# Kernel optimization log

Measured on AMD Instinct MI355X. Metric: run time of the kernel, lower is better.

Reference implementation:

```python
import jax, jax.numpy as jnp
import numpy as np

N = 50000
E = 1600000
IN_CH = 34
HID = 64
OUT = 64
NEG_SLOPE = 0.2


def _gat_layer(x, src, dst, W, a_src, a_dst, bias, heads, out_ch, concat):
    n = x.shape[0]
    xw = (x @ W).reshape(n, heads, out_ch)                      # [N,H,C]
    al_src = jnp.sum(xw * a_src[None], axis=-1)                  # [N,H]
    al_dst = jnp.sum(xw * a_dst[None], axis=-1)                  # [N,H]
    e = jax.nn.leaky_relu(al_src[src] + al_dst[dst], NEG_SLOPE)  # [E,H]
    # segment softmax over incoming edges of each dst node (self-loops ensure non-empty)
    m = jax.ops.segment_max(e, dst, num_segments=n)              # [N,H]
    ex = jnp.exp(e - m[dst])
    denom = jax.ops.segment_sum(ex, dst, num_segments=n)         # [N,H]
    alpha = ex / denom[dst]                                      # [E,H]
    msg = xw[src] * alpha[:, :, None]                            # [E,H,C]
    out = jax.ops.segment_sum(msg, dst, num_segments=n)          # [N,H,C]
    if concat:
        out = out.reshape(n, heads * out_ch)
    else:
        out = out.mean(axis=1)
    return out + bias


def setup_inputs() -> dict:
    key = jax.random.key(0)
    ks = jax.random.split(key, 12)
    x = jax.random.normal(ks[0], (N, IN_CH), dtype=jnp.float32)
    edge_index = jax.random.randint(ks[1], (2, E), 0, N, dtype=jnp.int64)
    # layer 1: heads=2, concat -> 128
    W1 = jax.random.normal(ks[2], (IN_CH, 2 * HID), dtype=jnp.float32) * 0.1
    a_src1 = jax.random.normal(ks[3], (2, HID), dtype=jnp.float32) * 0.1
    a_dst1 = jax.random.normal(ks[4], (2, HID), dtype=jnp.float32) * 0.1
    b1 = jnp.zeros((2 * HID,), dtype=jnp.float32)
    # layer 2: heads=1, mean
    W2 = jax.random.normal(ks[5], (2 * HID, OUT), dtype=jnp.float32) * 0.1
    a_src2 = jax.random.normal(ks[6], (1, OUT), dtype=jnp.float32) * 0.1
    a_dst2 = jax.random.normal(ks[7], (1, OUT), dtype=jnp.float32) * 0.1
    b2 = jnp.zeros((OUT,), dtype=jnp.float32)
    return {"x": x, "edge_index": edge_index, "W1": W1, "a_src1": a_src1,
            "a_dst1": a_dst1, "b1": b1, "W2": W2, "a_src2": a_src2,
            "a_dst2": a_dst2, "b2": b2}


def reference(x, edge_index, W1, a_src1, a_dst1, b1, W2, a_src2, a_dst2, b2):
    n = x.shape[0]
    loops = jnp.arange(n, dtype=edge_index.dtype)
    src = jnp.concatenate([edge_index[0], loops])  # PyG GATConv add_self_loops=True
    dst = jnp.concatenate([edge_index[1], loops])
    h = _gat_layer(x, src, dst, W1, a_src1, a_dst1, b1, heads=2, out_ch=HID, concat=True)
    h = jax.nn.relu(h)
    out = _gat_layer(h, src, dst, W2, a_src2, a_dst2, b2, heads=1, out_ch=OUT, concat=False)
    return out
```

## Files before the change

kernel.cpp:

```cpp
#include <hip/hip_runtime.h>
#include <math.h>

#define N_NODES 50000
#define E_EDGES 1600000
#define IN_CH   34
#define NEG     0.2f
#define NB      196
#define CAP     10000

typedef __attribute__((ext_vector_type(2))) float fv2;

static __device__ __forceinline__ unsigned short f2bf(float f) {
    unsigned int u = __float_as_uint(f);
    u += 0x7fffu + ((u >> 16) & 1u);
    return (unsigned short)(u >> 16);
}
static __device__ __forceinline__ float bflo(unsigned int u) {
    return __uint_as_float(u << 16);
}
static __device__ __forceinline__ float bfhi(unsigned int u) {
    return __uint_as_float(u & 0xffff0000u);
}
static __device__ __forceinline__ float lrelu_exp(float e) {
    return expf(e > 0.f ? e : NEG * e);
}

static __device__ __forceinline__ int scan256_excl(int v, int* wsum) {
    const int lane = threadIdx.x & 63, wv = threadIdx.x >> 6;
    int x = v;
    #pragma unroll
    for (int off = 1; off < 64; off <<= 1) {
        int y = __shfl_up(x, off);
        if (lane >= off) x += y;
    }
    if (lane == 63) wsum[wv] = x;
    __syncthreads();
    if (threadIdx.x < 4) {
        int s = wsum[threadIdx.x];
        #pragma unroll
        for (int off = 1; off < 4; off <<= 1) {
            int y = __shfl_up(s, off);
            if ((int)threadIdx.x >= off) s += y;
        }
        wsum[threadIdx.x] = s;
    }
    __syncthreads();
    const int woff = wv ? wsum[wv - 1] : 0;
    return woff + x - v;
}

__global__ __launch_bounds__(256) void k_bin(
    const int* __restrict__ srcA, const int* __restrict__ dstA,
    int* __restrict__ gcur, unsigned int* __restrict__ binned)
{
    __shared__ unsigned int raw[4096];
    __shared__ unsigned short rnk[4096];
    __shared__ int cnt[256], cur[256];
    const int tid = threadIdx.x;
    cnt[tid] = 0;
    __syncthreads();
    const int base = blockIdx.x * 4096;
    #pragma unroll
    for (int i = 0; i < 16; ++i) {
        const int e = base + i * 256 + tid;
        if (e < E_EDGES) {
            const int d = dstA[e], s = srcA[e];
            raw[i * 256 + tid] = ((unsigned int)d << 16) | (unsigned int)s;
            rnk[i * 256 + tid] = (unsigned short)atomicAdd(&cnt[d >> 8], 1);
        }
    }
    __syncthreads();
    const int v = cnt[tid];
    cur[tid] = (tid < NB && v > 0) ? (tid * CAP + atomicAdd(&gcur[tid], v)) : 0;
    __syncthreads();
    const int mE = min(4096, E_EDGES - base);
    for (int p = tid; p < mE; p += 256) {
        const unsigned int u = raw[p];
        binned[cur[u >> 24] + rnk[p]] = u;
    }
}

__global__ __launch_bounds__(256) void k_fine(
    const int* __restrict__ gcur, const unsigned int* __restrict__ binned,
    int2* __restrict__ rowspan, unsigned short* __restrict__ sorted_src)
{
    __shared__ unsigned int sbin[CAP];
    __shared__ unsigned short rnk[CAP];
    __shared__ int cnt[256], sbase[256];
    __shared__ int wsum[4];
    const int tid = threadIdx.x;
    const int b = blockIdx.x;
    const int bbase = b * CAP;
    const int cntb = gcur[b];
    cnt[tid] = 0;
    __syncthreads();
    for (int p = tid; p < cntb; p += 256) {
        const unsigned int u = binned[bbase + p];
        sbin[p] = u;
        rnk[p] = (unsigned short)atomicAdd(&cnt[(u >> 16) & 255], 1);
    }
    __syncthreads();
    const int v = cnt[tid];
    const int excl = scan256_excl(v, wsum);
    const int node = b * 256 + tid;
    if (node < N_NODES) rowspan[node] = make_int2(bbase + excl, bbase + excl + v);
    sbase[tid] = excl;
    __syncthreads();
    for (int p = tid; p < cntb; p += 256) {
        const unsigned int u = sbin[p];
        sorted_src[bbase + sbase[(u >> 16) & 255] + rnk[p]] =
            (unsigned short)(u & 0xffffu);
    }
}

__global__ __launch_bounds__(256) void k_node1(
    const float* __restrict__ x, const float* __restrict__ W1,
    const float* __restrict__ a_src, const float* __restrict__ a_dst,
    unsigned short* __restrict__ xw1b,
    float* __restrict__ al_s, float* __restrict__ al_d)
{
    __shared__ float sW[IN_CH * 132];
    __shared__ float sx[32 * 35];
    __shared__ float sas[128], sad[128];
    const int tid = threadIdx.x;
    for (int i = tid; i < IN_CH * 128; i += 256) {
        int k = i >> 7, c = i & 127;
        sW[k * 132 + c] = W1[i];
    }
    if (tid < 128) { sas[tid] = a_src[tid]; sad[tid] = a_dst[tid]; }
    const int n0 = blockIdx.x * 32;
    for (int i = tid; i < 32 * IN_CH; i += 256) {
        int n = i / IN_CH;
        sx[n * 35 + (i - n * IN_CH)] = (n0 + n < N_NODES) ? x[n0 * IN_CH + i] : 0.f;
    }
    __syncthreads();

    const int tc = tid & 31, tn = tid >> 5;
    float acc[4][4] = {{0.f}};
    for (int k = 0; k < IN_CH; ++k) {
        const float4 wv = *reinterpret_cast<const float4*>(&sW[k * 132 + 4 * tc]);
        #pragma unroll
        for (int j = 0; j < 4; ++j) {
            const float hj = sx[(4 * tn + j) * 35 + k];
            acc[j][0] += hj * wv.x; acc[j][1] += hj * wv.y;
            acc[j][2] += hj * wv.z; acc[j][3] += hj * wv.w;
        }
    }
    #pragma unroll
    for (int j = 0; j < 4; ++j) {
        const int node = n0 + 4 * tn + j;
        float ps = 0.f, pd = 0.f;
        #pragma unroll
        for (int c = 0; c < 4; ++c) {
            ps += acc[j][c] * sas[4 * tc + c];
            pd += acc[j][c] * sad[4 * tc + c];
        }
        #pragma unroll
        for (int off = 1; off < 16; off <<= 1) {
            ps += __shfl_xor(ps, off);
            pd += __shfl_xor(pd, off);
        }
        if (node < N_NODES) {
            if ((tc & 15) == 0) {
                int h = tc >> 4;
                al_s[node * 2 + h] = ps;
                al_d[node * 2 + h] = pd;
            }
            ushort4 u;
            u.x = f2bf(acc[j][0]); u.y = f2bf(acc[j][1]);
            u.z = f2bf(acc[j][2]); u.w = f2bf(acc[j][3]);
            *reinterpret_cast<ushort4*>(&xw1b[node * 128 + 4 * tc]) = u;
        }
    }
}

__global__ __launch_bounds__(256) void k_gather1(
    const int2* __restrict__ rowspan, const unsigned short* __restrict__ sorted_src,
    const unsigned int* __restrict__ xw1u,
    const float* __restrict__ al_s, const float* __restrict__ al_d,
    const float* __restrict__ b1, float* __restrict__ hbuf)
{
    __shared__ float4 AB[2][4][32];
    const int wave = threadIdx.x >> 6;
    const int lane = threadIdx.x & 63;
    const int node = blockIdx.x * 4 + wave;
    const int2 span = rowspan[node];
    const int head = lane >> 5;

    const float2 ald  = *reinterpret_cast<const float2*>(&al_d[node * 2]);
    const float2 als0 = *reinterpret_cast<const float2*>(&al_s[node * 2]);
    const float w0h0 = lrelu_exp(als0.x + ald.x);
    const float w0h1 = lrelu_exp(als0.y + ald.y);
    const float wself = head ? w0h1 : w0h0;

    const unsigned int su = xw1u[node * 64 + lane];
    fv2 accX = { wself * bflo(su), wself * bfhi(su) };
    fv2 accY = { 0.f, 0.f };
    float dv0 = 0.f, dv1 = 0.f;
    const float4* ABh = AB[head][wave];

    for (int base = span.x; base < span.y; base += 64) {
        const int rem = span.y - base;
        const int m = rem < 64 ? rem : 64;
        const int mp = (m + 1) & ~1;
        if (lane < m) {
            const int s = sorted_src[base + lane];
            const float2 als = *reinterpret_cast<const float2*>(&al_s[s * 2]);
            const float w0 = lrelu_exp(als.x + ald.x);
            const float w1 = lrelu_exp(als.y + ald.y);
            dv0 += w0; dv1 += w1;
            const float offf = __int_as_float(s << 6);
            ((float2*)&AB[0][wave][lane >> 1])[lane & 1] = make_float2(offf, w0);
            ((float2*)&AB[1][wave][lane >> 1])[lane & 1] = make_float2(offf, w1);
        } else if (lane < mp) {
            const float offf = __int_as_float(node << 6);
            ((float2*)&AB[0][wave][lane >> 1])[lane & 1] = make_float2(offf, 0.f);
            ((float2*)&AB[1][wave][lane >> 1])[lane & 1] = make_float2(offf, 0.f);
        }
        const int P = mp >> 1;
        int p = 0;
        for (; p + 8 <= P; p += 8) {
            float4 q[8];
            #pragma unroll
            for (int t = 0; t < 8; ++t) q[t] = ABh[p + t];
            unsigned int va[8], vb[8];
            #pragma unroll
            for (int t = 0; t < 8; ++t) {
                va[t] = xw1u[__float_as_int(q[t].x) + lane];
                vb[t] = xw1u[__float_as_int(q[t].z) + lane];
            }
            #pragma unroll
            for (int t = 0; t < 8; ++t) {
                fv2 f;
                f.x = bflo(va[t]); f.y = bfhi(va[t]); accX += f * q[t].y;
                f.x = bflo(vb[t]); f.y = bfhi(vb[t]); accY += f * q[t].w;
            }
        }
        for (; p < P; ++p) {
            const float4 q = ABh[p];
            const unsigned int a = xw1u[__float_as_int(q.x) + lane];
            const unsigned int b = xw1u[__float_as_int(q.z) + lane];
            fv2 f;
            f.x = bflo(a); f.y = bfhi(a); accX += f * q.y;
            f.x = bflo(b); f.y = bfhi(b); accY += f * q.w;
        }
    }
    accX += accY;
    #pragma unroll
    for (int off = 32; off; off >>= 1) {
        dv0 += __shfl_xor(dv0, off);
        dv1 += __shfl_xor(dv1, off);
    }
    const float den = head ? (dv1 + w0h1) : (dv0 + w0h0);
    const float2 bv = *reinterpret_cast<const float2*>(&b1[2 * lane]);
    float o0 = accX.x / den + bv.x;
    float o1 = accX.y / den + bv.y;
    o0 = o0 > 0.f ? o0 : 0.f;
    o1 = o1 > 0.f ? o1 : 0.f;
    *reinterpret_cast<float2*>(&hbuf[node * 128 + 2 * lane]) = make_float2(o0, o1);
}

__global__ __launch_bounds__(256) void k_node2(
    const float* __restrict__ hbuf, const float* __restrict__ W2,
    const float* __restrict__ a_src, const float* __restrict__ a_dst,
    unsigned short* __restrict__ xw2b, float* __restrict__ al_s, float* __restrict__ al_d)
{
    __shared__ float sW[128 * 64];
    __shared__ float sh[64 * 129];
    __shared__ float sas[64], sad[64];
    const int tid = threadIdx.x;
    for (int i = tid; i < 128 * 64; i += 256) sW[i] = W2[i];
    if (tid < 64) { sas[tid] = a_src[tid]; sad[tid] = a_dst[tid]; }
    const int n0 = blockIdx.x * 64;
    for (int i = tid; i < 64 * 128; i += 256) {
        int n = i >> 7, c = i & 127;
        sh[n * 129 + c] = (n0 + n < N_NODES) ? hbuf[(long)(n0 + n) * 128 + c] : 0.f;
    }
    __syncthreads();

    const int tc = tid & 15, tn = tid >> 4;
    float acc[4][4] = {{0.f}};
    for (int k = 0; k < 128; ++k) {
        const float4 wv = *reinterpret_cast<const float4*>(&sW[k * 64 + 4 * tc]);
        #pragma unroll
        for (int j = 0; j < 4; ++j) {
            const float hj = sh[(4 * tn + j) * 129 + k];
            acc[j][0] += hj * wv.x; acc[j][1] += hj * wv.y;
            acc[j][2] += hj * wv.z; acc[j][3] += hj * wv.w;
        }
    }
    #pragma unroll
    for (int j = 0; j < 4; ++j) {
        const int node = n0 + 4 * tn + j;
        float ps = 0.f, pd = 0.f;
        #pragma unroll
        for (int c = 0; c < 4; ++c) {
            ps += acc[j][c] * sas[4 * tc + c];
            pd += acc[j][c] * sad[4 * tc + c];
        }
        #pragma unroll
        for (int off = 1; off < 16; off <<= 1) {
            ps += __shfl_xor(ps, off);
            pd += __shfl_xor(pd, off);
        }
        if (node < N_NODES) {
            if (tc == 0) { al_s[node] = ps; al_d[node] = pd; }
            ushort4 u;
            u.x = f2bf(acc[j][0]); u.y = f2bf(acc[j][1]);
            u.z = f2bf(acc[j][2]); u.w = f2bf(acc[j][3]);
            *reinterpret_cast<ushort4*>(&xw2b[node * 64 + 4 * tc]) = u;
        }
    }
}

__global__ __launch_bounds__(256) void k_gather2(
    const int2* __restrict__ rowspan, const unsigned short* __restrict__ sorted_src,
    const unsigned int* __restrict__ xw2u,
    const float* __restrict__ al_s, const float* __restrict__ al_d,
    const float* __restrict__ b2, float* __restrict__ out)
{
    __shared__ float4 AB[4][32];
    const int wave = threadIdx.x >> 6;
    const int lane = threadIdx.x & 63;
    const int node = blockIdx.x * 4 + wave;
    const int2 span = rowspan[node];
    const int li = lane & 31, hsel = lane >> 5;

    const float ald = al_d[node];
    const float w0s = lrelu_exp(al_s[node] + ald);
    const unsigned int su = xw2u[node * 32 + li];
    const float wself = hsel ? 0.f : w0s;
    fv2 acc = { wself * bflo(su), wself * bfhi(su) };
    float dv = 0.f;
    const float4* ABw = AB[wave];

    for (int base = span.x; base < span.y; base += 64) {
        const int rem = span.y - base;
        const int m = rem < 64 ? rem : 64;
        const int mp = (m + 3) & ~3;
        if (lane < m) {
            const int s = sorted_src[base + lane];
            const float w = lrelu_exp(al_s[s] + ald);
            dv += w;
            ((float2*)&AB[wave][lane >> 1])[lane & 1] =
                make_float2(__int_as_float(s << 5), w);
        } else if (lane < mp) {
            ((float2*)&AB[wave][lane >> 1])[lane & 1] =
                make_float2(__int_as_float(node << 5), 0.f);
        }
        const int P = mp >> 1;
        int p = hsel;
        for (; p + 6 < P; p += 8) {
            float4 q[4];
            q[0] = ABw[p];     q[1] = ABw[p + 2];
            q[2] = ABw[p + 4]; q[3] = ABw[p + 6];
            unsigned int va[4], vb[4];
            #pragma unroll
            for (int t = 0; t < 4; ++t) {
                va[t] = xw2u[__float_as_int(q[t].x) + li];
                vb[t] = xw2u[__float_as_int(q[t].z) + li];
            }
            #pragma unroll
            for (int t = 0; t < 4; ++t) {
                fv2 f;
                f.x = bflo(va[t]); f.y = bfhi(va[t]); acc += f * q[t].y;
                f.x = bflo(vb[t]); f.y = bfhi(vb[t]); acc += f * q[t].w;
            }
        }
        for (; p < P; p += 2) {
            const float4 q = ABw[p];
            const unsigned int a = xw2u[__float_as_int(q.x) + li];
            const unsigned int b = xw2u[__float_as_int(q.z) + li];
            fv2 f;
            f.x = bflo(a); f.y = bfhi(a); acc += f * q.y;
            f.x = bflo(b); f.y = bfhi(b); acc += f * q.w;
        }
    }
    acc.x += __shfl_xor(acc.x, 32);
    acc.y += __shfl_xor(acc.y, 32);
    #pragma unroll
    for (int off = 32; off; off >>= 1) dv += __shfl_xor(dv, off);
    if (lane < 32) {
        const float den = dv + w0s;
        const float2 bv = *reinterpret_cast<const float2*>(&b2[2 * li]);
        *reinterpret_cast<float2*>(&out[node * 64 + 2 * li]) =
            make_float2(acc.x / den + bv.x, acc.y / den + bv.y);
    }
}

extern "C" void kernel_launch(void* const* d_in, const int* in_sizes, int n_in,
                              void* d_out, int out_size, void* d_ws, size_t ws_size,
                              hipStream_t stream)
{
    const float* x   = (const float*)d_in[0];
    const int*   ei  = (const int*)d_in[1];
    const float* W1  = (const float*)d_in[2];
    const float* as1 = (const float*)d_in[3];
    const float* ad1 = (const float*)d_in[4];
    const float* b1  = (const float*)d_in[5];
    const float* W2  = (const float*)d_in[6];
    const float* as2 = (const float*)d_in[7];
    const float* ad2 = (const float*)d_in[8];
    const float* b2  = (const float*)d_in[9];
    float* out = (float*)d_out;

    const int* srcA = ei;
    const int* dstA = ei + E_EDGES;

    char* ws = (char*)d_ws;
    int2*           rowspan    = (int2*)(ws);
    unsigned short* sorted_src = (unsigned short*)(ws + 409600);
    int*            gcur       = (int*)(ws + 4341760);
    float*          al_s1      = (float*)(ws + 4343808);
    float*          al_d1      = (float*)(ws + 4753408);
    float*          al_s2      = (float*)(ws + 5163008);
    float*          al_d2      = (float*)(ws + 5367808);
    unsigned short* xw1b       = (unsigned short*)(ws + 5572608);
    unsigned int*   binned     = (unsigned int*)(ws + 18376704);
    unsigned short* xw2b       = (unsigned short*)(ws + 26220544);
    float*          hbuf       = (float*)(ws + 32624640);

    hipMemsetAsync(gcur, 0, NB * sizeof(int), stream);
    hipLaunchKernelGGL(k_bin, dim3((E_EDGES + 4095) / 4096), dim3(256), 0, stream,
                       srcA, dstA, gcur, binned);
    hipLaunchKernelGGL(k_node1, dim3((N_NODES + 31) / 32), dim3(256), 0, stream,
                       x, W1, as1, ad1, xw1b, al_s1, al_d1);
    hipLaunchKernelGGL(k_fine, dim3(NB), dim3(256), 0, stream,
                       gcur, binned, rowspan, sorted_src);
    hipLaunchKernelGGL(k_gather1, dim3(N_NODES / 4), dim3(256), 0, stream,
                       rowspan, sorted_src, (const unsigned int*)xw1b,
                       al_s1, al_d1, b1, hbuf);
    hipLaunchKernelGGL(k_node2, dim3((N_NODES + 63) / 64), dim3(256), 0, stream,
                       hbuf, W2, as2, ad2, xw2b, al_s2, al_d2);
    hipLaunchKernelGGL(k_gather2, dim3(N_NODES / 4), dim3(256), 0, stream,
                       rowspan, sorted_src, (const unsigned int*)xw2b,
                       al_s2, al_d2, b2, out);
}
```

Before: 281.9 us.

## Split gather kernels across column slices so each wave covers more edges in parallel

```diff
diff --git a/kernel.cpp b/kernel.cpp
--- a/kernel.cpp
+++ b/kernel.cpp
@@ -180,84 +180,76 @@
     const float* __restrict__ al_s, const float* __restrict__ al_d,
     const float* __restrict__ b1, float* __restrict__ hbuf)
 {
-    __shared__ float4 AB[2][4][32];
+    __shared__ float2 eb[4][64];
     const int wave = threadIdx.x >> 6;
     const int lane = threadIdx.x & 63;
-    const int node = blockIdx.x * 4 + wave;
+    const int cs   = blockIdx.x & 3;
+    const int node = (blockIdx.x >> 2) * 4 + wave;
     const int2 span = rowspan[node];
-    const int head = lane >> 5;
-
-    const float2 ald  = *reinterpret_cast<const float2*>(&al_d[node * 2]);
-    const float2 als0 = *reinterpret_cast<const float2*>(&al_s[node * 2]);
-    const float w0h0 = lrelu_exp(als0.x + ald.x);
-    const float w0h1 = lrelu_exp(als0.y + ald.y);
-    const float wself = head ? w0h1 : w0h0;
-
-    const unsigned int su = xw1u[node * 64 + lane];
-    fv2 accX = { wself * bflo(su), wself * bfhi(su) };
-    fv2 accY = { 0.f, 0.f };
-    float dv0 = 0.f, dv1 = 0.f;
-    const float4* ABh = AB[head][wave];
+    const int h  = cs >> 1;
+    const int ul = lane & 15, ei = lane >> 4;
+    const int ubase = cs * 16 + ul;
+
+    const float ald = al_d[node * 2 + h];
+    const float w0 = lrelu_exp(al_s[node * 2 + h] + ald);
+    fv2 acc = { 0.f, 0.f };
+    if (ei == 0) {
+        const unsigned int su = xw1u[node * 64 + ubase];
+        acc.x = w0 * bflo(su); acc.y = w0 * bfhi(su);
+    }
+    float dv = 0.f;
+    float2* ebw = eb[wave];
 
     for (int base = span.x; base < span.y; base += 64) {
         const int rem = span.y - base;
         const int m = rem < 64 ? rem : 64;
-        const int mp = (m + 1) & ~1;
+        const int mp = (m + 3) & ~3;
         if (lane < m) {
             const int s = sorted_src[base + lane];
-            const float2 als = *reinterpret_cast<const float2*>(&al_s[s * 2]);
-            const float w0 = lrelu_exp(als.x + ald.x);
-            const float w1 = lrelu_exp(als.y + ald.y);
-            dv0 += w0; dv1 += w1;
-            const float offf = __int_as_float(s << 6);
-            ((float2*)&AB[0][wave][lane >> 1])[lane & 1] = make_float2(offf, w0);
-            ((float2*)&AB[1][wave][lane >> 1])[lane & 1] = make_float2(offf, w1);
+            const float w = lrelu_exp(al_s[s * 2 + h] + ald);
+            dv += w;
+            ebw[lane] = make_float2(__int_as_float(s << 6), w);
         } else if (lane < mp) {
-            const float offf = __int_as_float(node << 6);
-            ((float2*)&AB[0][wave][lane >> 1])[lane & 1] = make_float2(offf, 0.f);
-            ((float2*)&AB[1][wave][lane >> 1])[lane & 1] = make_float2(offf, 0.f);
-        }
-        const int P = mp >> 1;
-        int p = 0;
-        for (; p + 8 <= P; p += 8) {
-            float4 q[8];
-            #pragma unroll
-            for (int t = 0; t < 8; ++t) q[t] = ABh[p + t];
-            unsigned int va[8], vb[8];
-            #pragma unroll
-            for (int t = 0; t < 8; ++t) {
-                va[t] = xw1u[__float_as_int(q[t].x) + lane];
-                vb[t] = xw1u[__float_as_int(q[t].z) + lane];
-            }
-            #pragma unroll
-            for (int t = 0; t < 8; ++t) {
-                fv2 f;
-                f.x = bflo(va[t]); f.y = bfhi(va[t]); accX += f * q[t].y;
-                f.x = bflo(vb[t]); f.y = bfhi(vb[t]); accY += f * q[t].w;
-            }
-        }
-        for (; p < P; ++p) {
-            const float4 q = ABh[p];
-            const unsigned int a = xw1u[__float_as_int(q.x) + lane];
-            const unsigned int b = xw1u[__float_as_int(q.z) + lane];
+            ebw[lane] = make_float2(__int_as_float(node << 6), 0.f);
+        }
+        const int steps = mp >> 2;
+        int k = 0;
+        for (; k + 4 <= steps; k += 4) {
+            const float2 q0 = ebw[(k + 0) * 4 + ei];
+            const float2 q1 = ebw[(k + 1) * 4 + ei];
+            const float2 q2 = ebw[(k + 2) * 4 + ei];
+            const float2 q3 = ebw[(k + 3) * 4 + ei];
+            const unsigned int v0 = xw1u[__float_as_int(q0.x) + ubase];
+            const unsigned int v1 = xw1u[__float_as_int(q1.x) + ubase];
+            const unsigned int v2 = xw1u[__float_as_int(q2.x) + ubase];
+            const unsigned int v3 = xw1u[__float_as_int(q3.x) + ubase];
             fv2 f;
-            f.x = bflo(a); f.y = bfhi(a); accX += f * q.y;
-            f.x = bflo(b); f.y = bfhi(b); accY += f * q.w;
-        }
-    }
-    accX += accY;
-    #pragma unroll
-    for (int off = 32; off; off >>= 1) {
-        dv0 += __shfl_xor(dv0, off);
-        dv1 += __shfl_xor(dv1, off);
-    }
-    const float den = head ? (dv1 + w0h1) : (dv0 + w0h0);
-    const float2 bv = *reinterpret_cast<const float2*>(&b1[2 * lane]);
-    float o0 = accX.x / den + bv.x;
-    float o1 = accX.y / den + bv.y;
-    o0 = o0 > 0.f ? o0 : 0.f;
-    o1 = o1 > 0.f ? o1 : 0.f;
-    *reinterpret_cast<float2*>(&hbuf[node * 128 + 2 * lane]) = make_float2(o0, o1);
+            f.x = bflo(v0); f.y = bfhi(v0); acc += f * q0.y;
+            f.x = bflo(v1); f.y = bfhi(v1); acc += f * q1.y;
+            f.x = bflo(v2); f.y = bfhi(v2); acc += f * q2.y;
+            f.x = bflo(v3); f.y = bfhi(v3); acc += f * q3.y;
+        }
+        for (; k < steps; ++k) {
+            const float2 q = ebw[k * 4 + ei];
+            const unsigned int v = xw1u[__float_as_int(q.x) + ubase];
+            fv2 f;
+            f.x = bflo(v); f.y = bfhi(v); acc += f * q.y;
+        }
+    }
+    acc.x += __shfl_xor(acc.x, 16); acc.y += __shfl_xor(acc.y, 16);
+    acc.x += __shfl_xor(acc.x, 32); acc.y += __shfl_xor(acc.y, 32);
+    #pragma unroll
+    for (int off = 32; off; off >>= 1) dv += __shfl_xor(dv, off);
+    const float den = dv + w0;
+    if (lane < 16) {
+        const float2 bv = *reinterpret_cast<const float2*>(&b1[2 * ubase]);
+        float o0 = acc.x / den + bv.x;
+        float o1 = acc.y / den + bv.y;
+        o0 = o0 > 0.f ? o0 : 0.f;
+        o1 = o1 > 0.f ? o1 : 0.f;
+        *reinterpret_cast<float2*>(&hbuf[node * 128 + 2 * ubase]) =
+            make_float2(o0, o1);
+    }
 }
 
 __global__ __launch_bounds__(256) void k_node2(
@@ -319,71 +311,70 @@
     const float* __restrict__ al_s, const float* __restrict__ al_d,
     const float* __restrict__ b2, float* __restrict__ out)
 {
-    __shared__ float4 AB[4][32];
+    __shared__ float2 eb[4][64];
     const int wave = threadIdx.x >> 6;
     const int lane = threadIdx.x & 63;
-    const int node = blockIdx.x * 4 + wave;
+    const int cs   = blockIdx.x & 3;
+    const int node = (blockIdx.x >> 2) * 4 + wave;
     const int2 span = rowspan[node];
-    const int li = lane & 31, hsel = lane >> 5;
+    const int ul = lane & 7, ei = lane >> 3;
+    const int ubase = cs * 8 + ul;
 
     const float ald = al_d[node];
-    const float w0s = lrelu_exp(al_s[node] + ald);
-    const unsigned int su = xw2u[node * 32 + li];
-    const float wself = hsel ? 0.f : w0s;
-    fv2 acc = { wself * bflo(su), wself * bfhi(su) };
+    const float w0 = lrelu_exp(al_s[node] + ald);
+    fv2 acc = { 0.f, 0.f };
+    if (ei == 0) {
+        const unsigned int su = xw2u[node * 32 + ubase];
+        acc.x = w0 * bflo(su); acc.y = w0 * bfhi(su);
+    }
     float dv = 0.f;
-    const float4* ABw = AB[wave];
+    float2* ebw = eb[wave];
 
     for (int base = span.x; base < span.y; base += 64) {
         const int rem = span.y - base;
         const int m = rem < 64 ? rem : 64;
-        const int mp = (m + 3) & ~3;
+        const int mp = (m + 7) & ~7;
         if (lane < m) {
             const int s = sorted_src[base + lane];
             const float w = lrelu_exp(al_s[s] + ald);
             dv += w;
-            ((float2*)&AB[wave][lane >> 1])[lane & 1] =
-                make_float2(__int_as_float(s << 5), w);
+            ebw[lane] = make_float2(__int_as_float(s << 5), w);
         } else if (lane < mp) {
-            ((float2*)&AB[wave][lane >> 1])[lane & 1] =
-                make_float2(__int_as_float(node << 5), 0.f);
-        }
-        const int P = mp >> 1;
-        int p = hsel;
-        for (; p + 6 < P; p += 8) {
-            float4 q[4];
-            q[0] = ABw[p];     q[1] = ABw[p + 2];
-            q[2] = ABw[p + 4]; q[3] = ABw[p + 6];
-            unsigned int va[4], vb[4];
-            #pragma unroll
-            for (int t = 0; t < 4; ++t) {
-                va[t] = xw2u[__float_as_int(q[t].x) + li];
-                vb[t] = xw2u[__float_as_int(q[t].z) + li];
-            }
-            #pragma unroll
-            for (int t = 0; t < 4; ++t) {
-                fv2 f;
-                f.x = bflo(va[t]); f.y = bfhi(va[t]); acc += f * q[t].y;
-                f.x = bflo(vb[t]); f.y = bfhi(vb[t]); acc += f * q[t].w;
-            }
-        }
-        for (; p < P; p += 2) {
-            const float4 q = ABw[p];
-            const unsigned int a = xw2u[__float_as_int(q.x) + li];
-            const unsigned int b = xw2u[__float_as_int(q.z) + li];
+            ebw[lane] = make_float2(__int_as_float(node << 5), 0.f);
+        }
+        const int steps = mp >> 3;
+        int k = 0;
+        for (; k + 4 <= steps; k += 4) {
+            const float2 q0 = ebw[(k + 0) * 8 + ei];
+            const float2 q1 = ebw[(k + 1) * 8 + ei];
+            const float2 q2 = ebw[(k + 2) * 8 + ei];
+            const float2 q3 = ebw[(k + 3) * 8 + ei];
+            const unsigned int v0 = xw2u[__float_as_int(q0.x) + ubase];
+            const unsigned int v1 = xw2u[__float_as_int(q1.x) + ubase];
+            const unsigned int v2 = xw2u[__float_as_int(q2.x) + ubase];
+            const unsigned int v3 = xw2u[__float_as_int(q3.x) + ubase];
             fv2 f;
-            f.x = bflo(a); f.y = bfhi(a); acc += f * q.y;
-            f.x = bflo(b); f.y = bfhi(b); acc += f * q.w;
-        }
-    }
-    acc.x += __shfl_xor(acc.x, 32);
-    acc.y += __shfl_xor(acc.y, 32);
+            f.x = bflo(v0); f.y = bfhi(v0); acc += f * q0.y;
+            f.x = bflo(v1); f.y = bfhi(v1); acc += f * q1.y;
+            f.x = bflo(v2); f.y = bfhi(v2); acc += f * q2.y;
+            f.x = bflo(v3); f.y = bfhi(v3); acc += f * q3.y;
+        }
+        for (; k < steps; ++k) {
+            const float2 q = ebw[k * 8 + ei];
+            const unsigned int v = xw2u[__float_as_int(q.x) + ubase];
+            fv2 f;
+            f.x = bflo(v); f.y = bfhi(v); acc += f * q.y;
+        }
+    }
+    acc.x += __shfl_xor(acc.x, 8);  acc.y += __shfl_xor(acc.y, 8);
+    acc.x += __shfl_xor(acc.x, 16); acc.y += __shfl_xor(acc.y, 16);
+    acc.x += __shfl_xor(acc.x, 32); acc.y += __shfl_xor(acc.y, 32);
     #pragma unroll
     for (int off = 32; off; off >>= 1) dv += __shfl_xor(dv, off);
-    if (lane < 32) {
-        const float den = dv + w0s;
-        const float2 bv = *reinterpret_cast<const float2*>(&b2[2 * li]);
-        *reinterpret_cast<float2*>(&out[node * 64 + 2 * li]) =
+    const float den = dv + w0;
+    if (lane < 8) {
+        const float2 bv = *reinterpret_cast<const float2*>(&b2[2 * ubase]);
+        *reinterpret_cast<float2*>(&out[node * 64 + 2 * ubase]) =
             make_float2(acc.x / den + bv.x, acc.y / den + bv.y);
     }
 }
@@ -427,12 +418,12 @@
                        x, W1, as1, ad1, xw1b, al_s1, al_d1);
     hipLaunchKernelGGL(k_fine, dim3(NB), dim3(256), 0, stream,
                        gcur, binned, rowspan, sorted_src);
-    hipLaunchKernelGGL(k_gather1, dim3(N_NODES / 4), dim3(256), 0, stream,
+    hipLaunchKernelGGL(k_gather1, dim3((N_NODES / 4) * 4), dim3(256), 0, stream,
                        rowspan, sorted_src, (const unsigned int*)xw1b,
                        al_s1, al_d1, b1, hbuf);
     hipLaunchKernelGGL(k_node2, dim3((N_NODES + 63) / 64), dim3(256), 0, stream,
                        hbuf, W2, as2, ad2, xw2b, al_s2, al_d2);
-    hipLaunchKernelGGL(k_gather2, dim3(N_NODES / 4), dim3(256), 0, stream,
+    hipLaunchKernelGGL(k_gather2, dim3((N_NODES / 4) * 4), dim3(256), 0, stream,
                        rowspan, sorted_src, (const unsigned int*)xw2b,
                        al_s2, al_d2, b2, out);
 }
```

New measurement: 395.7 us. 40.4% more time.

## Fuse edge binning and layer-1 node transform into one launch; shrink gather unrolls

Applied to the files above, without the earlier changes.

```diff
diff --git a/kernel.cpp b/kernel.cpp
--- a/kernel.cpp
+++ b/kernel.cpp
@@ -7,6 +7,7 @@
 #define NEG     0.2f
 #define NB      196
 #define CAP     10000
+#define NBB     391
 
 typedef __attribute__((ext_vector_type(2))) float fv2;
 
@@ -49,34 +50,97 @@
     return woff + x - v;
 }
 
-__global__ __launch_bounds__(256) void k_bin(
+__global__ __launch_bounds__(256, 4) void k_bin_node1(
     const int* __restrict__ srcA, const int* __restrict__ dstA,
-    int* __restrict__ gcur, unsigned int* __restrict__ binned)
-{
-    __shared__ unsigned int raw[4096];
-    __shared__ unsigned short rnk[4096];
-    __shared__ int cnt[256], cur[256];
+    int* __restrict__ gcur, unsigned int* __restrict__ binned,
+    const float* __restrict__ x, const float* __restrict__ W1,
+    const float* __restrict__ a_src, const float* __restrict__ a_dst,
+    unsigned short* __restrict__ xw1b,
+    float* __restrict__ al_s, float* __restrict__ al_d)
+{
+    __shared__ __align__(16) char sm[26624];
     const int tid = threadIdx.x;
-    cnt[tid] = 0;
-    __syncthreads();
-    const int base = blockIdx.x * 4096;
-    #pragma unroll
-    for (int i = 0; i < 16; ++i) {
-        const int e = base + i * 256 + tid;
-        if (e < E_EDGES) {
-            const int d = dstA[e], s = srcA[e];
-            raw[i * 256 + tid] = ((unsigned int)d << 16) | (unsigned int)s;
-            rnk[i * 256 + tid] = (unsigned short)atomicAdd(&cnt[d >> 8], 1);
-        }
-    }
-    __syncthreads();
-    const int v = cnt[tid];
-    cur[tid] = (tid < NB && v > 0) ? (tid * CAP + atomicAdd(&gcur[tid], v)) : 0;
-    __syncthreads();
-    const int mE = min(4096, E_EDGES - base);
-    for (int p = tid; p < mE; p += 256) {
-        const unsigned int u = raw[p];
-        binned[cur[u >> 24] + rnk[p]] = u;
+
+    if (blockIdx.x < NBB) {
+        unsigned int*   raw = (unsigned int*)sm;
+        unsigned short* rnk = (unsigned short*)(sm + 16384);
+        int* cnt = (int*)(sm + 24576);
+        int* cur = (int*)(sm + 25600);
+        cnt[tid] = 0;
+        __syncthreads();
+        const int base = blockIdx.x * 4096;
+        #pragma unroll
+        for (int i = 0; i < 16; ++i) {
+            const int e = base + i * 256 + tid;
+            if (e < E_EDGES) {
+                const int d = dstA[e], s = srcA[e];
+                raw[i * 256 + tid] = ((unsigned int)d << 16) | (unsigned int)s;
+                rnk[i * 256 + tid] = (unsigned short)atomicAdd(&cnt[d >> 8], 1);
+            }
+        }
+        __syncthreads();
+        const int v = cnt[tid];
+        cur[tid] = (tid < NB && v > 0) ? (tid * CAP + atomicAdd(&gcur[tid], v)) : 0;
+        __syncthreads();
+        const int mE = min(4096, E_EDGES - base);
+        for (int p = tid; p < mE; p += 256) {
+            const unsigned int u = raw[p];
+            binned[cur[u >> 24] + rnk[p]] = u;
+        }
+    } else {
+        float* sW  = (float*)sm;
+        float* sx  = (float*)(sm + 17952);
+        float* sas = (float*)(sm + 22432);
+        float* sad = (float*)(sm + 22944);
+        for (int i = tid; i < IN_CH * 128; i += 256) {
+            int k = i >> 7, c = i & 127;
+            sW[k * 132 + c] = W1[i];
+        }
+        if (tid < 128) { sas[tid] = a_src[tid]; sad[tid] = a_dst[tid]; }
+        const int n0 = (blockIdx.x - NBB) * 32;
+        for (int i = tid; i < 32 * IN_CH; i += 256) {
+            int n = i / IN_CH;
+            sx[n * 35 + (i - n * IN_CH)] = (n0 + n < N_NODES) ? x[n0 * IN_CH + i] : 0.f;
+        }
+        __syncthreads();
+
+        const int tc = tid & 31, tn = tid >> 5;
+        float acc[4][4] = {{0.f}};
+        for (int k = 0; k < IN_CH; ++k) {
+            const float4 wv = *reinterpret_cast<const float4*>(&sW[k * 132 + 4 * tc]);
+            #pragma unroll
+            for (int j = 0; j < 4; ++j) {
+                const float hj = sx[(4 * tn + j) * 35 + k];
+                acc[j][0] += hj * wv.x; acc[j][1] += hj * wv.y;
+                acc[j][2] += hj * wv.z; acc[j][3] += hj * wv.w;
+            }
+        }
+        #pragma unroll
+        for (int j = 0; j < 4; ++j) {
+            const int node = n0 + 4 * tn + j;
+            float ps = 0.f, pd = 0.f;
+            #pragma unroll
+            for (int c = 0; c < 4; ++c) {
+                ps += acc[j][c] * sas[4 * tc + c];
+                pd += acc[j][c] * sad[4 * tc + c];
+            }
+            #pragma unroll
+            for (int off = 1; off < 16; off <<= 1) {
+                ps += __shfl_xor(ps, off);
+                pd += __shfl_xor(pd, off);
+            }
+            if (node < N_NODES) {
+                if ((tc & 15) == 0) {
+                    int h = tc >> 4;
+                    al_s[node * 2 + h] = ps;
+                    al_d[node * 2 + h] = pd;
+                }
+                ushort4 u;
+                u.x = f2bf(acc[j][0]); u.y = f2bf(acc[j][1]);
+                u.z = f2bf(acc[j][2]); u.w = f2bf(acc[j][3]);
+                *reinterpret_cast<ushort4*>(&xw1b[node * 128 + 4 * tc]) = u;
+            }
+        }
     }
 }
 
@@ -110,67 +174,6 @@
         const unsigned int u = sbin[p];
         sorted_src[bbase + sbase[(u >> 16) & 255] + rnk[p]] =
             (unsigned short)(u & 0xffffu);
-    }
-}
-
-__global__ __launch_bounds__(256) void k_node1(
-    const float* __restrict__ x, const float* __restrict__ W1,
-    const float* __restrict__ a_src, const float* __restrict__ a_dst,
-    unsigned short* __restrict__ xw1b,
-    float* __restrict__ al_s, float* __restrict__ al_d)
-{
-    __shared__ float sW[IN_CH * 132];
-    __shared__ float sx[32 * 35];
-    __shared__ float sas[128], sad[128];
-    const int tid = threadIdx.x;
-    for (int i = tid; i < IN_CH * 128; i += 256) {
-        int k = i >> 7, c = i & 127;
-        sW[k * 132 + c] = W1[i];
-    }
-    if (tid < 128) { sas[tid] = a_src[tid]; sad[tid] = a_dst[tid]; }
-    const int n0 = blockIdx.x * 32;
-    for (int i = tid; i < 32 * IN_CH; i += 256) {
-        int n = i / IN_CH;
-        sx[n * 35 + (i - n * IN_CH)] = (n0 + n < N_NODES) ? x[n0 * IN_CH + i] : 0.f;
-    }
-    __syncthreads();
-
-    const int tc = tid & 31, tn = tid >> 5;
-    float acc[4][4] = {{0.f}};
-    for (int k = 0; k < IN_CH; ++k) {
-        const float4 wv = *reinterpret_cast<const float4*>(&sW[k * 132 + 4 * tc]);
-        #pragma unroll
-        for (int j = 0; j < 4; ++j) {
-            const float hj = sx[(4 * tn + j) * 35 + k];
-            acc[j][0] += hj * wv.x; acc[j][1] += hj * wv.y;
-            acc[j][2] += hj * wv.z; acc[j][3] += hj * wv.w;
-        }
-    }
-    #pragma unroll
-    for (int j = 0; j < 4; ++j) {
-        const int node = n0 + 4 * tn + j;
-        float ps = 0.f, pd = 0.f;
-        #pragma unroll
-        for (int c = 0; c < 4; ++c) {
-            ps += acc[j][c] * sas[4 * tc + c];
-            pd += acc[j][c] * sad[4 * tc + c];
-        }
-        #pragma unroll
-        for (int off = 1; off < 16; off <<= 1) {
-            ps += __shfl_xor(ps, off);
-            pd += __shfl_xor(pd, off);
-        }
-        if (node < N_NODES) {
-            if ((tc & 15) == 0) {
-                int h = tc >> 4;
-                al_s[node * 2 + h] = ps;
-                al_d[node * 2 + h] = pd;
-            }
-            ushort4 u;
-            u.x = f2bf(acc[j][0]); u.y = f2bf(acc[j][1]);
-            u.z = f2bf(acc[j][2]); u.w = f2bf(acc[j][3]);
-            *reinterpret_cast<ushort4*>(&xw1b[node * 128 + 4 * tc]) = u;
-        }
     }
 }
 
@@ -219,22 +222,28 @@
         }
         const int P = mp >> 1;
         int p = 0;
-        for (; p + 8 <= P; p += 8) {
-            float4 q[8];
-            #pragma unroll
-            for (int t = 0; t < 8; ++t) q[t] = ABh[p + t];
-            unsigned int va[8], vb[8];
-            #pragma unroll
-            for (int t = 0; t < 8; ++t) {
-                va[t] = xw1u[__float_as_int(q[t].x) + lane];
-                vb[t] = xw1u[__float_as_int(q[t].z) + lane];
-            }
-            #pragma unroll
-            for (int t = 0; t < 8; ++t) {
-                fv2 f;
-                f.x = bflo(va[t]); f.y = bfhi(va[t]); accX += f * q[t].y;
-                f.x = bflo(vb[t]); f.y = bfhi(vb[t]); accY += f * q[t].w;
-            }
+        for (; p + 4 <= P; p += 4) {
+            const float4 q0 = ABh[p + 0];
+            const float4 q1 = ABh[p + 1];
+            const float4 q2 = ABh[p + 2];
+            const float4 q3 = ABh[p + 3];
+            const unsigned int a0 = xw1u[__float_as_int(q0.x) + lane];
+            const unsigned int b0 = xw1u[__float_as_int(q0.z) + lane];
+            const unsigned int a1 = xw1u[__float_as_int(q1.x) + lane];
+            const unsigned int b1v = xw1u[__float_as_int(q1.z) + lane];
+            const unsigned int a2 = xw1u[__float_as_int(q2.x) + lane];
+            const unsigned int b2 = xw1u[__float_as_int(q2.z) + lane];
+            const unsigned int a3 = xw1u[__float_as_int(q3.x) + lane];
+            const unsigned int b3 = xw1u[__float_as_int(q3.z) + lane];
+            fv2 f;
+            f.x = bflo(a0); f.y = bfhi(a0); accX += f * q0.y;
+            f.x = bflo(b0); f.y = bfhi(b0); accY += f * q0.w;
+            f.x = bflo(a1); f.y = bfhi(a1); accX += f * q1.y;
+            f.x = bflo(b1v); f.y = bfhi(b1v); accY += f * q1.w;
+            f.x = bflo(a2); f.y = bfhi(a2); accX += f * q2.y;
+            f.x = bflo(b2); f.y = bfhi(b2); accY += f * q2.w;
+            f.x = bflo(a3); f.y = bfhi(a3); accX += f * q3.y;
+            f.x = bflo(b3); f.y = bfhi(b3); accY += f * q3.w;
         }
         for (; p < P; ++p) {
             const float4 q = ABh[p];
@@ -350,22 +359,18 @@
         }
         const int P = mp >> 1;
         int p = hsel;
-        for (; p + 6 < P; p += 8) {
-            float4 q[4];
-            q[0] = ABw[p];     q[1] = ABw[p + 2];
-            q[2] = ABw[p + 4]; q[3] = ABw[p + 6];
-            unsigned int va[4], vb[4];
-            #pragma unroll
-            for (int t = 0; t < 4; ++t) {
-                va[t] = xw2u[__float_as_int(q[t].x) + li];
-                vb[t] = xw2u[__float_as_int(q[t].z) + li];
-            }
-            #pragma unroll
-            for (int t = 0; t < 4; ++t) {
-                fv2 f;
-                f.x = bflo(va[t]); f.y = bfhi(va[t]); acc += f * q[t].y;
-                f.x = bflo(vb[t]); f.y = bfhi(vb[t]); acc += f * q[t].w;
-            }
+        for (; p + 2 < P; p += 4) {
+            const float4 qA = ABw[p];
+            const float4 qB = ABw[p + 2];
+            const unsigned int aA = xw2u[__float_as_int(qA.x) + li];
+            const unsigned int bA = xw2u[__float_as_int(qA.z) + li];
+            const unsigned int aB = xw2u[__float_as_int(qB.x) + li];
+            const unsigned int bB = xw2u[__float_as_int(qB.z) + li];
+            fv2 f;
+            f.x = bflo(aA); f.y = bfhi(aA); acc += f * qA.y;
+            f.x = bflo(bA); f.y = bfhi(bA); acc += f * qA.w;
+            f.x = bflo(aB); f.y = bfhi(aB); acc += f * qB.y;
+            f.x = bflo(bB); f.y = bfhi(bB); acc += f * qB.w;
         }
         for (; p < P; p += 2) {
             const float4 q = ABw[p];
@@ -421,9 +426,8 @@
     float*          hbuf       = (float*)(ws + 32624640);
 
     hipMemsetAsync(gcur, 0, NB * sizeof(int), stream);
-    hipLaunchKernelGGL(k_bin, dim3((E_EDGES + 4095) / 4096), dim3(256), 0, stream,
-                       srcA, dstA, gcur, binned);
-    hipLaunchKernelGGL(k_node1, dim3((N_NODES + 31) / 32), dim3(256), 0, stream,
+    hipLaunchKernelGGL(k_bin_node1, dim3(NBB + (N_NODES + 31) / 32), dim3(256), 0, stream,
+                       srcA, dstA, gcur, binned,
                        x, W1, as1, ad1, xw1b, al_s1, al_d1);
     hipLaunchKernelGGL(k_fine, dim3(NB), dim3(256), 0, stream,
                        gcur, binned, rowspan, sorted_src);
```

Result: slower. 353.2 us (+25.3%).
